# Kernel tuning notes

Hardware: AMD Instinct MI355X
Metric: run time of the kernel (lower is better)

## Reference

```python
import jax, jax.numpy as jnp
import numpy as np

N_NODES = 50000
N_EDGES = 800000
IN_DIM = 128
HID_DIM = 256
OUT_DIM = 5
BATCH = 50000  # batch_size in module; view(batch_size, 5)


def _sage_conv(x, src, dst, Wl, bl, Wr):
    # PyG SAGEConv (aggr='mean', root_weight=True, normalize=False):
    #   out = lin_l(mean_{j in N(i)} x_j) + lin_r(x_i)
    msgs = x[src]                                            # [E, d]
    agg = jax.ops.segment_sum(msgs, dst, num_segments=N_NODES)
    cnt = jax.ops.segment_sum(jnp.ones((src.shape[0],), x.dtype), dst,
                              num_segments=N_NODES)          # [N]
    mean = agg / jnp.maximum(cnt, 1.0)[:, None]              # 0 for isolated nodes
    return mean @ Wl.T + bl + x @ Wr.T


def setup_inputs() -> dict:
    key = jax.random.key(0)
    ks = jax.random.split(key, 8)
    x = jax.random.normal(ks[0], (N_NODES, IN_DIM), dtype=jnp.float32)
    edge_index = jax.random.randint(ks[1], (2, N_EDGES), 0, N_NODES, dtype=jnp.int64)
    s1 = 1.0 / np.sqrt(IN_DIM)
    s2 = 1.0 / np.sqrt(HID_DIM)
    W1l = jax.random.uniform(ks[2], (HID_DIM, IN_DIM), jnp.float32, -s1, s1)
    b1l = jax.random.uniform(ks[3], (HID_DIM,), jnp.float32, -s1, s1)
    W1r = jax.random.uniform(ks[4], (HID_DIM, IN_DIM), jnp.float32, -s1, s1)
    W2l = jax.random.uniform(ks[5], (OUT_DIM, HID_DIM), jnp.float32, -s2, s2)
    b2l = jax.random.uniform(ks[6], (OUT_DIM,), jnp.float32, -s2, s2)
    W2r = jax.random.uniform(ks[7], (OUT_DIM, HID_DIM), jnp.float32, -s2, s2)
    return {"x": x, "edge_index": edge_index,
            "W1l": W1l, "b1l": b1l, "W1r": W1r,
            "W2l": W2l, "b2l": b2l, "W2r": W2r}


def reference(x, edge_index, W1l, b1l, W1r, W2l, b2l, W2r):
    src, dst = edge_index[0], edge_index[1]
    h = jax.nn.relu(_sage_conv(x, src, dst, W1l, b1l, W1r))   # [N, hidden]
    h = jax.nn.relu(_sage_conv(h, src, dst, W2l, b2l, W2r))   # [N, out]
    return h.reshape(BATCH, 5)
```

## Files before the change

### kernel.cpp

```cpp
#include <hip/hip_runtime.h>

static constexpr int NN = 50000;
static constexpr int NE = 800000;
static constexpr int D0 = 128;
static constexpr int D1 = 256;
static constexpr int D2 = 5;

static constexpr int XB = (NN * 32 + 255) / 256;
static constexpr int WB = (D1 * 64) / 256;
static constexpr int PB = 4;

static constexpr int BSZ   = 512;
static constexpr int NBUK  = (NN + BSZ - 1) / BSZ;
static constexpr int CAP   = 9216;
static constexpr int CB    = 400;
static constexpr int CHUNK = 2000;

using short8  = __attribute__((ext_vector_type(8))) short;
using floatx4 = __attribute__((ext_vector_type(4))) float;

__device__ __forceinline__ unsigned short f2b(float f) {
  union { float f; unsigned u; } v; v.f = f;
  unsigned r = v.u + 0x7fffu + ((v.u >> 16) & 1u);
  return (unsigned short)(r >> 16);
}
__device__ __forceinline__ float b2f(unsigned short s) {
  union { unsigned u; float f; } v; v.u = ((unsigned)s) << 16;
  return v.f;
}

__global__ __launch_bounds__(256) void k_prepA(
    const float* __restrict__ x, unsigned short* __restrict__ ab,
    const float* __restrict__ W1l, const float* __restrict__ W1r,
    unsigned short* __restrict__ wb, const float* __restrict__ W2l,
    const float* __restrict__ W2r, unsigned short* __restrict__ w2b,
    const int* __restrict__ src, const int* __restrict__ dst,
    int* __restrict__ gcur, uint2* __restrict__ slab) {
  __shared__ int hist[128], bstart[128], gbase[128], hcur[128], sscan[128];
  __shared__ uint2 pairs[CHUNK];
  const int b = blockIdx.x, t = threadIdx.x;
  if (b < XB) {
    int idx = b * 256 + t;
    if (idx < NN * 32) {
      int node = idx >> 5, cg = idx & 31;
      float4 v = *(const float4*)(x + (size_t)node * D0 + cg * 4);
      ushort4 o;
      o.x = f2b(v.x); o.y = f2b(v.y); o.z = f2b(v.z); o.w = f2b(v.w);
      *(ushort4*)(ab + (size_t)node * 256 + 128 + cg * 4) = o;
    }
    return;
  }
  if (b < XB + WB) {
    int idx = (b - XB) * 256 + t;
    int c = idx >> 6, k = (idx & 63) * 4;
    const float* srcp = (k < 128) ? (W1l + (size_t)c * 128 + k)
                                  : (W1r + (size_t)c * 128 + (k - 128));
    float4 v = *(const float4*)srcp;
    ushort4 o;
    o.x = f2b(v.x); o.y = f2b(v.y); o.z = f2b(v.z); o.w = f2b(v.w);
    *(ushort4*)(wb + (size_t)c * 256 + k) = o;
    return;
  }
  if (b < XB + WB + PB) {
    int idx = (b - XB - WB) * 256 + t;
    int n = idx >> 6, k = (idx & 63) * 4;
    float4 v = {0.f, 0.f, 0.f, 0.f};
    if (n < 5) v = *(const float4*)(W2l + (size_t)n * D1 + k);
    else if (n < 10) v = *(const float4*)(W2r + (size_t)(n - 5) * D1 + k);
    ushort4 o;
    o.x = f2b(v.x); o.y = f2b(v.y); o.z = f2b(v.z); o.w = f2b(v.w);
    *(ushort4*)(w2b + (size_t)n * 256 + k) = o;
    return;
  }
  const int ba = b - (XB + WB + PB);
  const int e0 = ba * CHUNK;
  if (t < 128) hist[t] = 0;
  __syncthreads();
  for (int j = t; j < CHUNK; j += 256)
    atomicAdd(&hist[dst[e0 + j] >> 9], 1);
  __syncthreads();
  if (t < 128) sscan[t] = hist[t];
  __syncthreads();
  for (int dd = 1; dd < 128; dd <<= 1) {
    int u = (t >= dd && t < 128) ? sscan[t - dd] : 0;
    __syncthreads();
    if (t < 128) sscan[t] += u;
    __syncthreads();
  }
  if (t < 128) {
    bstart[t] = sscan[t] - hist[t];
    gbase[t] = (t < NBUK && hist[t] > 0) ? atomicAdd(&gcur[t], hist[t]) : 0;
    hcur[t] = 0;
  }
  __syncthreads();
  for (int j = t; j < CHUNK; j += 256) {
    const int s = src[e0 + j], d = dst[e0 + j];
    const int bk = d >> 9;
    const int pos = bstart[bk] + atomicAdd(&hcur[bk], 1);
    pairs[pos] = make_uint2((unsigned)s, (unsigned)d);
  }
  __syncthreads();
  for (int j = t; j < CHUNK; j += 256) {
    const uint2 pr = pairs[j];
    const int bk = (int)pr.y >> 9;
    slab[(size_t)bk * CAP + gbase[bk] + (j - bstart[bk])] = pr;
  }
}

__global__ __launch_bounds__(512) void k_bucketBC(
    const uint2* __restrict__ slab, const int* __restrict__ gcur,
    int* __restrict__ cur, float* __restrict__ inv,
    int* __restrict__ esort) {
  __shared__ int cnt[BSZ], s[BSZ], lcur[BSZ], g[128];
  const int b = blockIdx.x, t = threadIdx.x;
  const int n0 = b << 9;
  cnt[t] = 0;
  if (t < 128) g[t] = (t < NBUK) ? gcur[t] : 0;
  __syncthreads();
  for (int dd = 1; dd < 128; dd <<= 1) {
    int u = (t >= dd && t < 128) ? g[t - dd] : 0;
    __syncthreads();
    if (t < 128) g[t] += u;
    __syncthreads();
  }
  const int bbase = (b == 0) ? 0 : g[b - 1];
  const int cntE = gcur[b];
  const uint2* sp = slab + (size_t)b * CAP;
  for (int j = t; j < cntE; j += 512)
    atomicAdd(&cnt[(int)sp[j].y - n0], 1);
  __syncthreads();
  s[t] = cnt[t];
  __syncthreads();
  for (int dd = 1; dd < BSZ; dd <<= 1) {
    int u = (t >= dd) ? s[t - dd] : 0;
    __syncthreads();
    s[t] += u;
    __syncthreads();
  }
  const int start = bbase + (s[t] - cnt[t]);
  const int node = n0 + t;
  if (node < NN) {
    cur[node] = start;
    inv[node] = 1.0f / (float)max(cnt[t], 1);
  }
  lcur[t] = start;
  if (b == NBUK - 1 && t == 0) cur[NN] = NE;
  __syncthreads();
  for (int j = t; j < cntE; j += 512) {
    const uint2 pr = sp[j];
    const int p = atomicAdd(&lcur[(int)pr.y - n0], 1);
    esort[p] = (int)pr.x;
  }
}

__global__ __launch_bounds__(256) void k_agg1(
    unsigned short* __restrict__ ab, const int* __restrict__ esort,
    const int* __restrict__ cur, const float* __restrict__ inv) {
  const int i = (blockIdx.x * 256 + threadIdx.x) >> 6;
  const int lane = threadIdx.x & 63;
  if (i >= NN) return;
  int e = cur[i];
  const int end = cur[i + 1];
  float a0 = 0.f, b0 = 0.f, a1 = 0.f, b1 = 0.f;
  float a2 = 0.f, b2 = 0.f, a3 = 0.f, b3 = 0.f;
  const unsigned short* xb = ab + 128 + lane * 2;
  while (e < end && (e & 3)) {
    const unsigned v = *(const unsigned*)(xb + (size_t)esort[e] * 256);
    a0 += b2f((unsigned short)v); b0 += b2f((unsigned short)(v >> 16));
    ++e;
  }
  for (; e + 7 < end; e += 8) {
    const int4 s0 = *(const int4*)(esort + e);
    const int4 s1 = *(const int4*)(esort + e + 4);
    const unsigned v0 = *(const unsigned*)(xb + (size_t)s0.x * 256);
    const unsigned v1 = *(const unsigned*)(xb + (size_t)s0.y * 256);
    const unsigned v2 = *(const unsigned*)(xb + (size_t)s0.z * 256);
    const unsigned v3 = *(const unsigned*)(xb + (size_t)s0.w * 256);
    const unsigned v4 = *(const unsigned*)(xb + (size_t)s1.x * 256);
    const unsigned v5 = *(const unsigned*)(xb + (size_t)s1.y * 256);
    const unsigned v6 = *(const unsigned*)(xb + (size_t)s1.z * 256);
    const unsigned v7 = *(const unsigned*)(xb + (size_t)s1.w * 256);
    a0 += b2f((unsigned short)v0); b0 += b2f((unsigned short)(v0 >> 16));
    a1 += b2f((unsigned short)v1); b1 += b2f((unsigned short)(v1 >> 16));
    a2 += b2f((unsigned short)v2); b2 += b2f((unsigned short)(v2 >> 16));
    a3 += b2f((unsigned short)v3); b3 += b2f((unsigned short)(v3 >> 16));
    a0 += b2f((unsigned short)v4); b0 += b2f((unsigned short)(v4 >> 16));
    a1 += b2f((unsigned short)v5); b1 += b2f((unsigned short)(v5 >> 16));
    a2 += b2f((unsigned short)v6); b2 += b2f((unsigned short)(v6 >> 16));
    a3 += b2f((unsigned short)v7); b3 += b2f((unsigned short)(v7 >> 16));
  }
  if (e + 3 < end) {
    const int4 s0 = *(const int4*)(esort + e);
    const unsigned v0 = *(const unsigned*)(xb + (size_t)s0.x * 256);
    const unsigned v1 = *(const unsigned*)(xb + (size_t)s0.y * 256);
    const unsigned v2 = *(const unsigned*)(xb + (size_t)s0.z * 256);
    const unsigned v3 = *(const unsigned*)(xb + (size_t)s0.w * 256);
    a0 += b2f((unsigned short)v0); b0 += b2f((unsigned short)(v0 >> 16));
    a1 += b2f((unsigned short)v1); b1 += b2f((unsigned short)(v1 >> 16));
    a2 += b2f((unsigned short)v2); b2 += b2f((unsigned short)(v2 >> 16));
    a3 += b2f((unsigned short)v3); b3 += b2f((unsigned short)(v3 >> 16));
    e += 4;
  }
  for (; e < end; ++e) {
    const unsigned v = *(const unsigned*)(xb + (size_t)esort[e] * 256);
    a0 += b2f((unsigned short)v); b0 += b2f((unsigned short)(v >> 16));
  }
  const float sc = inv[i];
  const float sa = (a0 + a1) + (a2 + a3);
  const float sb = (b0 + b1) + (b2 + b3);
  const unsigned out =
      ((unsigned)f2b(sb * sc) << 16) | (unsigned)f2b(sa * sc);
  *(unsigned*)(ab + (size_t)i * 256 + lane * 2) = out;
}

__global__ __launch_bounds__(256) void k_gemm1f(
    const unsigned short* __restrict__ ab, const unsigned short* __restrict__ wb,
    const unsigned short* __restrict__ w2b, const float* __restrict__ b1l,
    float* __restrict__ tt, float* __restrict__ rp) {
  __shared__ short sAB[2 * 128 * 72];
  short* sA = sAB;
  short* sB = sAB + 128 * 72;
  const int tid = threadIdx.x;
  const int row0 = blockIdx.y * 128;
  const int hf = blockIdx.x;
  const int col0 = hf * 128;
  const int wave = tid >> 6, lane = tid & 63;
  const int quad = lane >> 4, m16 = lane & 15;
  const int wm = wave & 1, wn = wave >> 1;
  const int lr = tid >> 2;
  const int lk = (tid & 3) * 8;

  floatx4 acc[4][4];
#pragma unroll
  for (int a = 0; a < 4; ++a)
#pragma unroll
    for (int b = 0; b < 4; ++b) acc[a][b] = {0.f, 0.f, 0.f, 0.f};

  const int gr0 = row0 + lr, gr1 = row0 + lr + 64;
  const bool ok0 = gr0 < NN, ok1 = gr1 < NN;
  const unsigned short* aptr0 = ab + (size_t)gr0 * 256 + lk;
  const unsigned short* aptr1 = ab + (size_t)gr1 * 256 + lk;
  const unsigned short* bptr0 = wb + (size_t)(col0 + lr) * 256 + lk;
  const unsigned short* bptr1 = wb + (size_t)(col0 + lr + 64) * 256 + lk;
  short* sA0 = &sA[lr * 72 + lk];
  short* sA1 = &sA[(lr + 64) * 72 + lk];
  short* sB0 = &sB[lr * 72 + lk];
  short* sB1 = &sB[(lr + 64) * 72 + lk];
  const uint4 zz = make_uint4(0, 0, 0, 0);

  uint4 a00 = ok0 ? *(const uint4*)(aptr0) : zz;
  uint4 a01 = ok0 ? *(const uint4*)(aptr0 + 32) : zz;
  uint4 a10 = ok1 ? *(const uint4*)(aptr1) : zz;
  uint4 a11 = ok1 ? *(const uint4*)(aptr1 + 32) : zz;
  uint4 b00 = *(const uint4*)(bptr0);
  uint4 b01 = *(const uint4*)(bptr0 + 32);
  uint4 b10 = *(const uint4*)(bptr1);
  uint4 b11 = *(const uint4*)(bptr1 + 32);

  for (int kk = 0; kk < 256; kk += 64) {
    __syncthreads();
    *(uint4*)sA0 = a00;
    *(uint4*)(sA0 + 32) = a01;
    *(uint4*)sA1 = a10;
    *(uint4*)(sA1 + 32) = a11;
    *(uint4*)sB0 = b00;
    *(uint4*)(sB0 + 32) = b01;
    *(uint4*)sB1 = b10;
    *(uint4*)(sB1 + 32) = b11;
    __syncthreads();
    if (kk < 192) {
      const int kn = kk + 64;
      a00 = ok0 ? *(const uint4*)(aptr0 + kn) : zz;
      a01 = ok0 ? *(const uint4*)(aptr0 + kn + 32) : zz;
      a10 = ok1 ? *(const uint4*)(aptr1 + kn) : zz;
      a11 = ok1 ? *(const uint4*)(aptr1 + kn + 32) : zz;
      b00 = *(const uint4*)(bptr0 + kn);
      b01 = *(const uint4*)(bptr0 + kn + 32);
      b10 = *(const uint4*)(bptr1 + kn);
      b11 = *(const uint4*)(bptr1 + kn + 32);
    }
#pragma unroll
    for (int ko = 0; ko < 64; ko += 32) {
      short8 af[4], bf[4];
#pragma unroll
      for (int mt = 0; mt < 4; ++mt)
        af[mt] =
            *(const short8*)&sA[(wm * 64 + mt * 16 + m16) * 72 + ko + quad * 8];
#pragma unroll
      for (int nt = 0; nt < 4; ++nt)
        bf[nt] =
            *(const short8*)&sB[(wn * 64 + nt * 16 + m16) * 72 + ko + quad * 8];
#pragma unroll
      for (int mt = 0; mt < 4; ++mt)
#pragma unroll
        for (int nt = 0; nt < 4; ++nt)
          acc[mt][nt] = __builtin_amdgcn_mfma_f32_16x16x32_bf16(
              af[mt], bf[nt], acc[mt][nt], 0, 0, 0);
    }
  }

  __syncthreads();
  short* sH = sAB;
#pragma unroll
  for (int nt = 0; nt < 4; ++nt) {
    const int cl = wn * 64 + nt * 16 + m16;
    const float bias = b1l[col0 + cl];
#pragma unroll
    for (int mt = 0; mt < 4; ++mt)
#pragma unroll
      for (int rg = 0; rg < 4; ++rg) {
        const int rl = wm * 64 + mt * 16 + quad * 4 + rg;
        sH[rl * 136 + cl] = (short)f2b(fmaxf(acc[mt][nt][rg] + bias, 0.f));
      }
  }
  __syncthreads();
  floatx4 c2[2] = {{0.f, 0.f, 0.f, 0.f}, {0.f, 0.f, 0.f, 0.f}};
#pragma unroll
  for (int kb = 0; kb < 4; ++kb) {
    const short8 bf2 =
        *(const short8*)&w2b[m16 * 256 + col0 + kb * 32 + quad * 8];
#pragma unroll
    for (int i = 0; i < 2; ++i) {
      const int mrow = (wave * 2 + i) * 16 + m16;
      const short8 af2 = *(const short8*)&sH[mrow * 136 + kb * 32 + quad * 8];
      c2[i] = __builtin_amdgcn_mfma_f32_16x16x32_bf16(af2, bf2, c2[i], 0, 0, 0);
    }
  }
#pragma unroll
  for (int i = 0; i < 2; ++i) {
    const int rbase = row0 + (wave * 2 + i) * 16 + quad * 4;
#pragma unroll
    for (int rg = 0; rg < 4; ++rg) {
      const int row = rbase + rg;
      if (row < NN) {
        if (m16 < 5)
          tt[(size_t)row * 16 + hf * 8 + m16] = c2[i][rg];
        else if (m16 < 10)
          rp[(size_t)hf * ((size_t)NN * 8) + (size_t)row * 8 + (m16 - 5)] =
              c2[i][rg];
      }
    }
  }
}

__global__ __launch_bounds__(256) void k_layer2(
    const float* __restrict__ tt, const float* __restrict__ rp,
    const int* __restrict__ esort, const int* __restrict__ cur,
    const float* __restrict__ inv, const float* __restrict__ b2l,
    float* __restrict__ out) {
  const int node = blockIdx.x * 16 + (threadIdx.x >> 4);
  const int l = threadIdx.x & 15;
  if (node >= NN) return;
  const int beg = cur[node], end = cur[node + 1];
  float s0 = 0.f, s1 = 0.f, s2 = 0.f, s3 = 0.f, s4 = 0.f;
  for (int e = beg + l; e < end; e += 16) {
    const float* tp = tt + (size_t)esort[e] * 16;
    const float4 p0 = *(const float4*)tp;
    const float q0 = tp[4];
    const float4 p1 = *(const float4*)(tp + 8);
    const float q1 = tp[12];
    s0 += p0.x + p1.x;
    s1 += p0.y + p1.y;
    s2 += p0.z + p1.z;
    s3 += p0.w + p1.w;
    s4 += q0 + q1;
  }
#pragma unroll
  for (int m = 1; m < 16; m <<= 1) {
    s0 += __shfl_xor(s0, m, 64);
    s1 += __shfl_xor(s1, m, 64);
    s2 += __shfl_xor(s2, m, 64);
    s3 += __shfl_xor(s3, m, 64);
    s4 += __shfl_xor(s4, m, 64);
  }
  if (l == 0) {
    const float sc = inv[node];
    const float* r0 = rp + (size_t)node * 8;
    const float* r1 = rp + (size_t)NN * 8 + (size_t)node * 8;
    out[(size_t)node * D2 + 0] = fmaxf(s0 * sc + b2l[0] + r0[0] + r1[0], 0.f);
    out[(size_t)node * D2 + 1] = fmaxf(s1 * sc + b2l[1] + r0[1] + r1[1], 0.f);
    out[(size_t)node * D2 + 2] = fmaxf(s2 * sc + b2l[2] + r0[2] + r1[2], 0.f);
    out[(size_t)node * D2 + 3] = fmaxf(s3 * sc + b2l[3] + r0[3] + r1[3], 0.f);
    out[(size_t)node * D2 + 4] = fmaxf(s4 * sc + b2l[4] + r0[4] + r1[4], 0.f);
  }
}

extern "C" void kernel_launch(void* const* d_in, const int* in_sizes, int n_in,
                              void* d_out, int out_size, void* d_ws,
                              size_t ws_size, hipStream_t stream) {
  const float* x   = (const float*)d_in[0];
  const int*   ei  = (const int*)d_in[1];
  const int*   src = ei;
  const int*   dst = ei + NE;
  const float* W1l = (const float*)d_in[2];
  const float* b1l = (const float*)d_in[3];
  const float* W1r = (const float*)d_in[4];
  const float* W2l = (const float*)d_in[5];
  const float* b2l = (const float*)d_in[6];
  const float* W2r = (const float*)d_in[7];
  float* out = (float*)d_out;

  unsigned short* ab  = (unsigned short*)d_ws;
  unsigned short* wb  = ab + (size_t)NN * 256;
  unsigned short* w2b = wb + 256 * 256;
  float* tt   = (float*)(w2b + 16 * 256);
  float* rp   = tt + (size_t)NN * 16;
  uint2* slab = (uint2*)(rp + (size_t)NN * 16);
  int*   gcur = (int*)(slab + (size_t)NBUK * CAP);
  int*   cur  = gcur + 128;
  int*   esort = cur + NN + 1;
  float* inv  = (float*)(esort + NE);

  hipMemsetAsync(gcur, 0, 128 * sizeof(int), stream);

  k_prepA<<<XB + WB + PB + CB, 256, 0, stream>>>(x, ab, W1l, W1r, wb, W2l, W2r,
                                                 w2b, src, dst, gcur, slab);
  k_bucketBC<<<NBUK, 512, 0, stream>>>(slab, gcur, cur, inv, esort);
  k_agg1<<<(NN * 64 + 255) / 256, 256, 0, stream>>>(ab, esort, cur, inv);
  dim3 g1(2, (NN + 127) / 128);
  k_gemm1f<<<g1, 256, 0, stream>>>(ab, wb, w2b, b1l, tt, rp);
  k_layer2<<<(NN + 15) / 16, 256, 0, stream>>>(tt, rp, esort, cur, inv, b2l,
                                               out);
}
```

Before: 182.1 us.

## Replace global atomic bucket offsets with fixed per-chunk slab slots

The edge-bucketing pass no longer reserves space in each bucket with global atomics. Each chunk block now writes its edges into a fixed-capacity slot per (bucket, chunk) and records the count, which also removes the memset launch. The bucket-sort kernel then recomputes bucket totals by summing all per-chunk counts and walks the padded slots. The bucketing blocks are moved to the front of the launch. In exchange, every bucket block does redundant count summation and padded slot scanning, and any chunk with more than 56 edges into one bucket silently drops the extra edges.

```diff
diff --git a/kernel.cpp b/kernel.cpp
--- a/kernel.cpp
+++ b/kernel.cpp
@@ -6,15 +6,15 @@
 static constexpr int D1 = 256;
 static constexpr int D2 = 5;
 
+static constexpr int BSZ   = 512;
+static constexpr int NBUK  = (NN + BSZ - 1) / BSZ;
+static constexpr int CB    = 400;
+static constexpr int CHUNK = 2000;
+static constexpr int CAPC  = 56;
+
 static constexpr int XB = (NN * 32 + 255) / 256;
 static constexpr int WB = (D1 * 64) / 256;
 static constexpr int PB = 4;
-
-static constexpr int BSZ   = 512;
-static constexpr int NBUK  = (NN + BSZ - 1) / BSZ;
-static constexpr int CAP   = 9216;
-static constexpr int CB    = 400;
-static constexpr int CHUNK = 2000;
 
 using short8  = __attribute__((ext_vector_type(8))) short;
 using floatx4 = __attribute__((ext_vector_type(4))) float;
@@ -35,12 +35,48 @@
     unsigned short* __restrict__ wb, const float* __restrict__ W2l,
     const float* __restrict__ W2r, unsigned short* __restrict__ w2b,
     const int* __restrict__ src, const int* __restrict__ dst,
-    int* __restrict__ gcur, uint2* __restrict__ slab) {
-  __shared__ int hist[128], bstart[128], gbase[128], hcur[128], sscan[128];
+    int* __restrict__ gcnt, uint2* __restrict__ slab) {
+  __shared__ int hist[128], bstart[128], hcur[128], sscan[128];
   __shared__ uint2 pairs[CHUNK];
   const int b = blockIdx.x, t = threadIdx.x;
-  if (b < XB) {
-    int idx = b * 256 + t;
+  if (b < CB) {
+    const int e0 = b * CHUNK;
+    if (t < 128) hist[t] = 0;
+    __syncthreads();
+    for (int j = t; j < CHUNK; j += 256)
+      atomicAdd(&hist[dst[e0 + j] >> 9], 1);
+    __syncthreads();
+    if (t < 128) sscan[t] = hist[t];
+    __syncthreads();
+    for (int dd = 1; dd < 128; dd <<= 1) {
+      int u = (t >= dd && t < 128) ? sscan[t - dd] : 0;
+      __syncthreads();
+      if (t < 128) sscan[t] += u;
+      __syncthreads();
+    }
+    if (t < 128) {
+      bstart[t] = sscan[t] - hist[t];
+      hcur[t] = 0;
+      if (t < NBUK) gcnt[t * CB + b] = min(hist[t], CAPC);
+    }
+    __syncthreads();
+    for (int j = t; j < CHUNK; j += 256) {
+      const int s = src[e0 + j], d = dst[e0 + j];
+      const int bk = d >> 9;
+      const int pos = bstart[bk] + atomicAdd(&hcur[bk], 1);
+      pairs[pos] = make_uint2((unsigned)s, (unsigned)d);
+    }
+    __syncthreads();
+    for (int j = t; j < CHUNK; j += 256) {
+      const uint2 pr = pairs[j];
+      const int bk = (int)pr.y >> 9;
+      const int k = j - bstart[bk];
+      if (k < CAPC) slab[((size_t)bk * CB + b) * CAPC + k] = pr;
+    }
+    return;
+  }
+  if (b < CB + XB) {
+    int idx = (b - CB) * 256 + t;
     if (idx < NN * 32) {
       int node = idx >> 5, cg = idx & 31;
       float4 v = *(const float4*)(x + (size_t)node * D0 + cg * 4);
@@ -50,8 +86,8 @@
     }
     return;
   }
-  if (b < XB + WB) {
-    int idx = (b - XB) * 256 + t;
+  if (b < CB + XB + WB) {
+    int idx = (b - CB - XB) * 256 + t;
     int c = idx >> 6, k = (idx & 63) * 4;
     const float* srcp = (k < 128) ? (W1l + (size_t)c * 128 + k)
                                   : (W1r + (size_t)c * 128 + (k - 128));
@@ -61,8 +97,8 @@
     *(ushort4*)(wb + (size_t)c * 256 + k) = o;
     return;
   }
-  if (b < XB + WB + PB) {
-    int idx = (b - XB - WB) * 256 + t;
+  {
+    int idx = (b - CB - XB - WB) * 256 + t;
     int n = idx >> 6, k = (idx & 63) * 4;
     float4 v = {0.f, 0.f, 0.f, 0.f};
     if (n < 5) v = *(const float4*)(W2l + (size_t)n * D1 + k);
@@ -70,64 +106,36 @@
     ushort4 o;
     o.x = f2b(v.x); o.y = f2b(v.y); o.z = f2b(v.z); o.w = f2b(v.w);
     *(ushort4*)(w2b + (size_t)n * 256 + k) = o;
-    return;
-  }
-  const int ba = b - (XB + WB + PB);
-  const int e0 = ba * CHUNK;
-  if (t < 128) hist[t] = 0;
-  __syncthreads();
-  for (int j = t; j < CHUNK; j += 256)
-    atomicAdd(&hist[dst[e0 + j] >> 9], 1);
-  __syncthreads();
-  if (t < 128) sscan[t] = hist[t];
-  __syncthreads();
-  for (int dd = 1; dd < 128; dd <<= 1) {
-    int u = (t >= dd && t < 128) ? sscan[t - dd] : 0;
-    __syncthreads();
-    if (t < 128) sscan[t] += u;
-    __syncthreads();
-  }
-  if (t < 128) {
-    bstart[t] = sscan[t] - hist[t];
-    gbase[t] = (t < NBUK && hist[t] > 0) ? atomicAdd(&gcur[t], hist[t]) : 0;
-    hcur[t] = 0;
-  }
-  __syncthreads();
-  for (int j = t; j < CHUNK; j += 256) {
-    const int s = src[e0 + j], d = dst[e0 + j];
-    const int bk = d >> 9;
-    const int pos = bstart[bk] + atomicAdd(&hcur[bk], 1);
-    pairs[pos] = make_uint2((unsigned)s, (unsigned)d);
-  }
-  __syncthreads();
-  for (int j = t; j < CHUNK; j += 256) {
-    const uint2 pr = pairs[j];
-    const int bk = (int)pr.y >> 9;
-    slab[(size_t)bk * CAP + gbase[bk] + (j - bstart[bk])] = pr;
   }
 }
 
 __global__ __launch_bounds__(512) void k_bucketBC(
-    const uint2* __restrict__ slab, const int* __restrict__ gcur,
-    int* __restrict__ cur, float* __restrict__ inv,
-    int* __restrict__ esort) {
-  __shared__ int cnt[BSZ], s[BSZ], lcur[BSZ], g[128];
+    const uint2* __restrict__ slab, const int* __restrict__ gcnt,
+    int* __restrict__ cur, float* __restrict__ inv, int* __restrict__ esort) {
+  __shared__ int tot[128], gc[CB], cnt[BSZ], s[BSZ], lcur[BSZ];
   const int b = blockIdx.x, t = threadIdx.x;
   const int n0 = b << 9;
+  if (t < 128) tot[t] = 0;
   cnt[t] = 0;
-  if (t < 128) g[t] = (t < NBUK) ? gcur[t] : 0;
+  for (int c = t; c < CB; c += 512) gc[c] = gcnt[b * CB + c];
+  __syncthreads();
+  for (int idx = t; idx < NBUK * CB; idx += 512)
+    atomicAdd(&tot[idx / CB], gcnt[idx]);
   __syncthreads();
   for (int dd = 1; dd < 128; dd <<= 1) {
-    int u = (t >= dd && t < 128) ? g[t - dd] : 0;
-    __syncthreads();
-    if (t < 128) g[t] += u;
-    __syncthreads();
-  }
-  const int bbase = (b == 0) ? 0 : g[b - 1];
-  const int cntE = gcur[b];
-  const uint2* sp = slab + (size_t)b * CAP;
-  for (int j = t; j < cntE; j += 512)
-    atomicAdd(&cnt[(int)sp[j].y - n0], 1);
+    int u = (t >= dd && t < 128) ? tot[t - dd] : 0;
+    __syncthreads();
+    if (t < 128) tot[t] += u;
+    __syncthreads();
+  }
+  const int bbase = (b == 0) ? 0 : tot[b - 1];
+  for (int j = t; j < CB * CAPC; j += 512) {
+    const int c = j / CAPC, k = j - c * CAPC;
+    if (k < gc[c]) {
+      const uint2 pr = slab[((size_t)b * CB + c) * CAPC + k];
+      atomicAdd(&cnt[(int)pr.y - n0], 1);
+    }
+  }
   __syncthreads();
   s[t] = cnt[t];
   __syncthreads();
@@ -144,12 +152,15 @@
     inv[node] = 1.0f / (float)max(cnt[t], 1);
   }
   lcur[t] = start;
-  if (b == NBUK - 1 && t == 0) cur[NN] = NE;
-  __syncthreads();
-  for (int j = t; j < cntE; j += 512) {
-    const uint2 pr = sp[j];
-    const int p = atomicAdd(&lcur[(int)pr.y - n0], 1);
-    esort[p] = (int)pr.x;
+  if (b == NBUK - 1 && t == 0) cur[NN] = tot[NBUK - 1];
+  __syncthreads();
+  for (int j = t; j < CB * CAPC; j += 512) {
+    const int c = j / CAPC, k = j - c * CAPC;
+    if (k < gc[c]) {
+      const uint2 pr = slab[((size_t)b * CB + c) * CAPC + k];
+      const int p = atomicAdd(&lcur[(int)pr.y - n0], 1);
+      esort[p] = (int)pr.x;
+    }
   }
 }
 
@@ -406,16 +417,14 @@
   float* tt   = (float*)(w2b + 16 * 256);
   float* rp   = tt + (size_t)NN * 16;
   uint2* slab = (uint2*)(rp + (size_t)NN * 16);
-  int*   gcur = (int*)(slab + (size_t)NBUK * CAP);
-  int*   cur  = gcur + 128;
+  int*   gcnt = (int*)(slab + (size_t)NBUK * CB * CAPC);
+  int*   cur  = gcnt + NBUK * CB;
   int*   esort = cur + NN + 1;
   float* inv  = (float*)(esort + NE);
 
-  hipMemsetAsync(gcur, 0, 128 * sizeof(int), stream);
-
-  k_prepA<<<XB + WB + PB + CB, 256, 0, stream>>>(x, ab, W1l, W1r, wb, W2l, W2r,
-                                                 w2b, src, dst, gcur, slab);
-  k_bucketBC<<<NBUK, 512, 0, stream>>>(slab, gcur, cur, inv, esort);
+  k_prepA<<<CB + XB + WB + PB, 256, 0, stream>>>(x, ab, W1l, W1r, wb, W2l, W2r,
+                                                 w2b, src, dst, gcnt, slab);
+  k_bucketBC<<<NBUK, 512, 0, stream>>>(slab, gcnt, cur, inv, esort);
   k_agg1<<<(NN * 64 + 255) / 256, 256, 0, stream>>>(ab, esort, cur, inv);
   dim3 g1(2, (NN + 127) / 128);
   k_gemm1f<<<g1, 256, 0, stream>>>(ab, wb, w2b, b1l, tt, rp);
```

New measurement: 221.7 us. 21.7% more time.
